# Performance work log

Hardware: AMD Instinct MI355X
Metric: run time of the kernel (lower is better)

The kernel has to match this reference:

```python
import jax, jax.numpy as jnp
import numpy as np

B, C, L, MID, HID, OUT, K = 4096, 6, 1024, 512, 512, 256, 5
EPS = 1e-5


def _bn_eval(x, g, b, m, v):
    # BatchNorm1d eval mode on (B, C, T): normalize per channel with running stats
    inv = g / jnp.sqrt(v + EPS)
    return (x - m[None, :, None]) * inv[None, :, None] + b[None, :, None]


def setup_inputs() -> dict:
    key = jax.random.key(0)
    ks = jax.random.split(key, 12)
    s_in = 1.0 / np.sqrt(L)
    s_hid = 1.0 / np.sqrt(HID)
    inp = {
        "x": jax.random.normal(ks[0], (B, C, L), jnp.float32),
        # k stacked self-attention branches (two Linear(L, MID) each)
        "aW1": jax.random.normal(ks[1], (K, L, MID), jnp.float32) * s_in,
        "ab1": jnp.zeros((K, MID), jnp.float32),
        "aW2": jax.random.normal(ks[2], (K, L, MID), jnp.float32) * s_in,
        "ab2": jnp.zeros((K, MID), jnp.float32),
        # linearExchangeLayer: Linear(K*C, C)
        "linW": jax.random.normal(ks[3], (K * C, C), jnp.float32) / np.sqrt(K * C),
        "linb": jnp.zeros((C,), jnp.float32),
        # GraphConvolution weights
        "gW1": jax.random.normal(ks[4], (L, HID), jnp.float32) * s_in,
        "gb1": jnp.zeros((HID,), jnp.float32),
        "gW2": jax.random.normal(ks[5], (HID, OUT), jnp.float32) * s_hid,
        "gb2": jnp.zeros((OUT,), jnp.float32),
        # PReLU (single shared parameter, torch default 0.25)
        "prelu_a": jnp.array(0.25, jnp.float32),
        # BatchNorm1d params + running stats (eval mode)
        "bn1_g": jnp.ones((C,), jnp.float32),
        "bn1_b": jnp.zeros((C,), jnp.float32),
        "bn1_m": jnp.zeros((C,), jnp.float32),
        "bn1_v": jnp.ones((C,), jnp.float32),
        "bn2_g": jnp.ones((C,), jnp.float32),
        "bn2_b": jnp.zeros((C,), jnp.float32),
        "bn2_m": jnp.zeros((C,), jnp.float32),
        "bn2_v": jnp.ones((C,), jnp.float32),
    }
    return inp


def reference(x, aW1, ab1, aW2, ab2, linW, linb, gW1, gb1, gW2, gb2,
              prelu_a, bn1_g, bn1_b, bn1_m, bn1_v, bn2_g, bn2_b, bn2_m, bn2_v):
    b, c, l = x.shape
    k = aW1.shape[0]
    # --- multi-head attention adjacency: (b, c, c) ---
    q = jnp.einsum('bcl,klm->bkcm', x, aW1) + ab1[None, :, None, :]
    kv = jnp.einsum('bcl,klm->bkcm', x, aW2) + ab2[None, :, None, :]
    scores = jax.nn.softmax(jnp.einsum('bkcm,bkdm->bkcd', q, kv), axis=-1)
    # concat heads along last dim: (b, c, k*c)
    cat = scores.transpose(0, 2, 1, 3).reshape(b, c, k * c)
    A = jax.nn.softmax(cat @ linW + linb, axis=-1)  # (b, c, c)
    # --- GraphConvolution 1 (dropout identity in eval) ---
    h = jnp.einsum('bcd,bdh->bch', A, x @ gW1) + gb1
    # PReLU then BatchNorm1d
    h = jnp.where(h >= 0, h, prelu_a * h)
    h = _bn_eval(h, bn1_g, bn1_b, bn1_m, bn1_v)
    # --- GraphConvolution 2 ---
    out = jnp.einsum('bcd,bdh->bch', A, h @ gW2) + gb2
    out = _bn_eval(out, bn2_g, bn2_b, bn2_m, bn2_v)
    return out
```

## Files before the change

### kernel.cpp

```cpp
#include <hip/hip_runtime.h>
#include <hip/hip_bf16.h>


using bf16 = __hip_bfloat16;
using s16x8 = __attribute__((ext_vector_type(8))) short;
using f32x4 = __attribute__((ext_vector_type(4))) float;

#define AS1(p) ((__attribute__((address_space(1))) void*)((void*)(p)))
#define AS3(p) ((__attribute__((address_space(3))) void*)(p))

#if defined(__has_builtin)
#if __has_builtin(__builtin_amdgcn_global_load_lds)
#define HAVE_GLL 1
#endif
#endif

__device__ __forceinline__ float s2f(short s) {
  union { unsigned int u; float f; } c;
  c.u = ((unsigned int)(unsigned short)s) << 16;
  return c.f;
}
__device__ __forceinline__ short f2s(float x) {
  bf16 b = __float2bfloat16(x);
  short s;
  __builtin_memcpy(&s, &b, 2);
  return s;
}

struct GJob {
  const bf16* Bt;
  const float* bias;
  int boff;
  bf16* out;
};

__global__ void cvt_f32_bf16(const float* __restrict__ in, bf16* __restrict__ out, int n8) {
  int i = blockIdx.x * blockDim.x + threadIdx.x;
  if (i >= n8) return;
  float4 p0 = ((const float4*)in)[i * 2];
  float4 p1 = ((const float4*)in)[i * 2 + 1];
  s16x8 v;
  v[0] = f2s(p0.x); v[1] = f2s(p0.y); v[2] = f2s(p0.z); v[3] = f2s(p0.w);
  v[4] = f2s(p1.x); v[5] = f2s(p1.y); v[6] = f2s(p1.z); v[7] = f2s(p1.w);
  ((s16x8*)out)[i] = v;
}

__global__ void transpose_f2b(const float* __restrict__ in, bf16* __restrict__ out,
                              int R, int C) {
  __shared__ short tile[32][33];
  const float* src = in + (size_t)blockIdx.z * R * C;
  short* dst = (short*)out + (size_t)blockIdx.z * R * C;
  int r0 = blockIdx.x * 32, c0 = blockIdx.y * 32;
  int tx = threadIdx.x, ty = threadIdx.y;
#pragma unroll
  for (int i = 0; i < 4; ++i)
    tile[ty + i * 8][tx] = f2s(src[(size_t)(r0 + ty + i * 8) * C + c0 + tx]);
  __syncthreads();
#pragma unroll
  for (int i = 0; i < 4; ++i)
    dst[(size_t)(c0 + ty + i * 8) * R + r0 + tx] = tile[tx][ty + i * 8];
}

template <int AF32>
__global__ __launch_bounds__(256) void gemm_bt(
    const void* __restrict__ Ag,
    const bf16* __restrict__ Bt0, const bf16* __restrict__ Bt1,
    const float* __restrict__ bias0, const float* __restrict__ bias1, int boff,
    bf16* __restrict__ out0, bf16* __restrict__ out1,
    int M, int N, int K) {
  const bf16* Bt = (blockIdx.z == 0) ? Bt0 : Bt1;
  const float* bias = (blockIdx.z == 0) ? bias0 : bias1;
  bf16* Cg = (blockIdx.z == 0) ? out0 : out1;

  __shared__ short lA[128 * 32];
  __shared__ short lB[128 * 32];

  const int tid = threadIdx.x;
  const int lane = tid & 63, w = tid >> 6;
  const int wr = w >> 1, wc = w & 1;
  const int l16 = lane & 15, quad = lane >> 4;
  const int lrow = lane >> 2;
  const int scol = (((lane & 3) ^ ((lane >> 3) & 3)) * 8);

  const size_t rm0 = (size_t)blockIdx.x * 128;
  const size_t cn0 = (size_t)blockIdx.y * 128;

  f32x4 acc[4][4];
#pragma unroll
  for (int i = 0; i < 4; ++i)
#pragma unroll
    for (int j = 0; j < 4; ++j) acc[i][j] = (f32x4){0.f, 0.f, 0.f, 0.f};

  for (int kb = 0; kb < K; kb += 32) {
#pragma unroll
    for (int t = 0; t < 2; ++t) {
      int chunk = w * 2 + t;
      int row = chunk * 16 + lrow;
      const bf16* gb = Bt + (cn0 + row) * (size_t)K + kb + scol;
#ifdef HAVE_GLL
      __builtin_amdgcn_global_load_lds(AS1(gb), AS3(lB + chunk * 512), 16, 0, 0);
#else
      *(s16x8*)(lB + chunk * 512 + lane * 8) = *(const s16x8*)gb;
#endif
      if (AF32) {
        const float* ga = (const float*)Ag + (rm0 + row) * (size_t)K + kb + scol;
        float4 p0 = *(const float4*)ga;
        float4 p1 = *(const float4*)(ga + 4);
        s16x8 v;
        v[0] = f2s(p0.x); v[1] = f2s(p0.y); v[2] = f2s(p0.z); v[3] = f2s(p0.w);
        v[4] = f2s(p1.x); v[5] = f2s(p1.y); v[6] = f2s(p1.z); v[7] = f2s(p1.w);
        *(s16x8*)(lA + chunk * 512 + lane * 8) = v;
      } else {
        const bf16* ga = (const bf16*)Ag + (rm0 + row) * (size_t)K + kb + scol;
#ifdef HAVE_GLL
        __builtin_amdgcn_global_load_lds(AS1(ga), AS3(lA + chunk * 512), 16, 0, 0);
#else
        *(s16x8*)(lA + chunk * 512 + lane * 8) = *(const s16x8*)ga;
#endif
      }
    }
    __syncthreads();

    const int q2 = (quad ^ ((l16 >> 1) & 3)) * 8;
    s16x8 af[4], bfv[4];
#pragma unroll
    for (int i = 0; i < 4; ++i) {
      af[i] = *(const s16x8*)(lA + (wr * 64 + i * 16 + l16) * 32 + q2);
      bfv[i] = *(const s16x8*)(lB + (wc * 64 + i * 16 + l16) * 32 + q2);
    }
#pragma unroll
    for (int i = 0; i < 4; ++i)
#pragma unroll
      for (int j = 0; j < 4; ++j)
        acc[i][j] = __builtin_amdgcn_mfma_f32_16x16x32_bf16(af[i], bfv[j], acc[i][j], 0, 0, 0);
    __syncthreads();
  }

#pragma unroll
  for (int j = 0; j < 4; ++j) {
    size_t col = cn0 + wc * 64 + j * 16 + l16;
    float bv = bias ? bias[boff + col] : 0.f;
#pragma unroll
    for (int i = 0; i < 4; ++i) {
      size_t rowb = rm0 + wr * 64 + i * 16 + quad * 4;
#pragma unroll
      for (int r = 0; r < 4; ++r) {
        float v = acc[i][j][r] + bv;
        Cg[(rowb + r) * (size_t)N + col] = __float2bfloat16(v);
      }
    }
  }
}

__global__ __launch_bounds__(512, 2) void gemm256_8ph(
    const bf16* __restrict__ A,
    GJob j0, GJob j1, GJob j2, GJob j3,
    int M, int N, int K) {
  const GJob j = (blockIdx.z == 0) ? j0 : (blockIdx.z == 1) ? j1
               : (blockIdx.z == 2) ? j2 : j3;
  const bf16* Bt = j.Bt;
  const float* bias = j.bias;
  const int boff = j.boff;
  bf16* Cg = j.out;

  __shared__ __attribute__((aligned(16))) short ldsS[65536];

  const int tid = threadIdx.x;
  const int w = tid >> 6, l = tid & 63;
  const int l16 = l & 15, quad = l >> 4;
  const int wr = w >> 2, wc = w & 3;

  const size_t rm0 = (size_t)blockIdx.x * 256;
  const size_t cn0 = (size_t)blockIdx.y * 256;

  const int colS = ((l & 7) ^ (l >> 3)) * 8;
  const int rowS = w * 16 + (l >> 3);
  const short* pAs = (const short*)A + (rm0 + rowS) * (size_t)K + colS;
  const short* pBs = (const short*)Bt + (cn0 + rowS) * (size_t)K + colS;

  const int u0 = (quad ^ (l16 & 7)) * 8;
  const int u1 = ((quad + 4) ^ (l16 & 7)) * 8;

  f32x4 acc[8][4];
#pragma unroll
  for (int i = 0; i < 8; ++i)
#pragma unroll
    for (int j2i = 0; j2i < 4; ++j2i) acc[i][j2i] = (f32x4){0.f, 0.f, 0.f, 0.f};

  s16x8 af[4][2], bf0[2][2], bf1[2][2];

  const int T = K >> 6;

#ifdef HAVE_GLL
#define SA(BUF, H, KB) do {                                                          \
    __builtin_amdgcn_global_load_lds(AS1(pAs + (size_t)((H) * 128) * K + (KB)),      \
        AS3(ldsS + (BUF) * 32768 + (H) * 8192 + w * 1024), 16, 0, 0);                \
    __builtin_amdgcn_global_load_lds(AS1(pAs + (size_t)((H) * 128 + 8) * K + (KB)),  \
        AS3(ldsS + (BUF) * 32768 + (H) * 8192 + w * 1024 + 512), 16, 0, 0);          \
  } while (0)
#define SB(BUF, H, KB) do {                                                          \
    __builtin_amdgcn_global_load_lds(AS1(pBs + (size_t)((H) * 128) * K + (KB)),      \
        AS3(ldsS + (BUF) * 32768 + 16384 + (H) * 8192 + w * 1024), 16, 0, 0);        \
    __builtin_amdgcn_global_load_lds(AS1(pBs + (size_t)((H) * 128 + 8) * K + (KB)),  \
        AS3(ldsS + (BUF) * 32768 + 16384 + (H) * 8192 + w * 1024 + 512), 16, 0, 0);  \
  } while (0)
#else
#define SA(BUF, H, KB) do {                                                          \
    *(s16x8*)(ldsS + (BUF) * 32768 + (H) * 8192 + w * 1024 + l * 8) =                \
        *(const s16x8*)(pAs + (size_t)((H) * 128) * K + (KB));                       \
    *(s16x8*)(ldsS + (BUF) * 32768 + (H) * 8192 + w * 1024 + 512 + l * 8) =          \
        *(const s16x8*)(pAs + (size_t)((H) * 128 + 8) * K + (KB));                   \
  } while (0)
#define SB(BUF, H, KB) do {                                                          \
    *(s16x8*)(ldsS + (BUF) * 32768 + 16384 + (H) * 8192 + w * 1024 + l * 8) =        \
        *(const s16x8*)(pBs + (size_t)((H) * 128) * K + (KB));                       \
    *(s16x8*)(ldsS + (BUF) * 32768 + 16384 + (H) * 8192 + w * 1024 + 512 + l * 8) =  \
        *(const s16x8*)(pBs + (size_t)((H) * 128 + 8) * K + (KB));                   \
  } while (0)
#endif

#define LDA(BUF, MH) do {                                                            \
    _Pragma("unroll") for (int i = 0; i < 4; ++i) {                                  \
      const short* bse = ldsS + (BUF) * 32768 + wr * 8192 + (MH) * 4096 +            \
                         i * 1024 + l16 * 64;                                        \
      af[i][0] = *(const s16x8*)(bse + u0);                                          \
      af[i][1] = *(const s16x8*)(bse + u1);                                          \
    }                                                                                \
  } while (0)

#define LDB(BUF, NH, DST) do {                                                       \
    _Pragma("unroll") for (int n = 0; n < 2; ++n) {                                  \
      const short* bse = ldsS + (BUF) * 32768 + 16384 + (wc >> 1) * 8192 +           \
                         (wc & 1) * 4096 + (NH) * 2048 + n * 1024 + l16 * 64;        \
      DST[n][0] = *(const s16x8*)(bse + u0);                                         \
      DST[n][1] = *(const s16x8*)(bse + u1);                                         \
    }                                                                                \
  } while (0)

#define MFMAQ(MH, NH, BSET) do {                                                     \
    _Pragma("unroll") for (int i = 0; i < 4; ++i)                                    \
      _Pragma("unroll") for (int n = 0; n < 2; ++n) {                                \
        acc[(MH) * 4 + i][(NH) * 2 + n] = __builtin_amdgcn_mfma_f32_16x16x32_bf16(   \
            af[i][0], BSET[n][0], acc[(MH) * 4 + i][(NH) * 2 + n], 0, 0, 0);         \
        acc[(MH) * 4 + i][(NH) * 2 + n] = __builtin_amdgcn_mfma_f32_16x16x32_bf16(   \
            af[i][1], BSET[n][1], acc[(MH) * 4 + i][(NH) * 2 + n], 0, 0, 0);         \
      }                                                                              \
  } while (0)

#define BARX() asm volatile("s_barrier" ::: "memory")
#define LGKM0() do { asm volatile("s_waitcnt lgkmcnt(0)" ::: "memory");              \
                     __builtin_amdgcn_sched_barrier(0); } while (0)
#define VM6() do { asm volatile("s_waitcnt vmcnt(6)" ::: "memory");                  \
                   __builtin_amdgcn_sched_barrier(0); } while (0)

#define TILE_STEP(BUF, t) do {                                                       \
    const int kN_ = ((t) + 1 < T ? (t) + 1 : T - 1) << 6;                            \
    const int k2_ = ((t) + 2 < T ? (t) + 2 : T - 1) << 6;                            \
               \
    LDA(BUF, 0); LDB(BUF, 0, bf0); LDB(BUF, 1, bf1);                                 \
    SA((BUF) ^ 1, 1, kN_);                                                           \
    BARX(); LGKM0();                                                                 \
    __builtin_amdgcn_s_setprio(1); MFMAQ(0, 0, bf0); __builtin_amdgcn_s_setprio(0);  \
    BARX();                                                                          \
                        \
    SB(BUF, 0, k2_);                                                                 \
    BARX();                                                                          \
    __builtin_amdgcn_s_setprio(1); MFMAQ(0, 1, bf1); __builtin_amdgcn_s_setprio(0);  \
    BARX();                                                                          \
                                               \
    LDA(BUF, 1);                                                                     \
    SB(BUF, 1, k2_);                                                                 \
    BARX(); LGKM0();                                                                 \
    __builtin_amdgcn_s_setprio(1); MFMAQ(1, 1, bf1); __builtin_amdgcn_s_setprio(0);  \
    BARX();                                                                          \
                         \
    SA(BUF, 0, k2_);                                                                 \
    VM6();                                                                           \
    BARX();                                                                          \
    __builtin_amdgcn_s_setprio(1); MFMAQ(1, 0, bf0); __builtin_amdgcn_s_setprio(0);  \
    BARX();                                                                          \
  } while (0)

  {
    const int k1_ = (T > 1 ? 1 : 0) << 6;
    SB(0, 0, 0); SB(0, 1, 0); SA(0, 0, 0); SA(0, 1, 0);
    SB(1, 0, k1_); SB(1, 1, k1_); SA(1, 0, k1_);
    VM6();
    BARX();
  }

  for (int t = 0; t < T; t += 2) {
    TILE_STEP(0, t);
    TILE_STEP(1, t + 1);
  }

#pragma unroll
  for (int jj = 0; jj < 4; ++jj) {
    size_t col = cn0 + wc * 64 + jj * 16 + l16;
    float bv = bias ? bias[boff + col] : 0.f;
#pragma unroll
    for (int i = 0; i < 8; ++i) {
      size_t rowb = rm0 + wr * 128 + i * 16 + quad * 4;
#pragma unroll
      for (int r = 0; r < 4; ++r) {
        Cg[(rowb + r) * (size_t)N + col] = __float2bfloat16(acc[i][jj][r] + bv);
      }
    }
  }
#undef SA
#undef SB
#undef LDA
#undef LDB
#undef MFMAQ
#undef BARX
#undef LGKM0
#undef VM6
#undef TILE_STEP
}

__global__ __launch_bounds__(256) void scores_mfma2(
    const bf16* __restrict__ Q0, const bf16* __restrict__ KV0,
    const bf16* __restrict__ Q1, const bf16* __restrict__ KV1,
    float* __restrict__ S, int head0) {
  const int h = blockIdx.y;
  const bf16* Q = h ? Q1 : Q0;
  const bf16* KV = h ? KV1 : KV0;
  const int head = head0 + h;

  const int tid = threadIdx.x;
  const int lane = tid & 63, w = tid >> 6;
  const int l16 = lane & 15, quad = lane >> 4;
  const int b0 = (blockIdx.x * 4 + w) * 2;

  int gr = (l16 < 8) ? (b0 * 6 + l16) : ((b0 + 1) * 6 + (l16 - 8));
  if (gr > 24575) gr = 24575;

  const short* qrow = (const short*)Q + (size_t)gr * 512 + quad * 8;
  const short* krow = (const short*)KV + (size_t)gr * 512 + quad * 8;

  f32x4 acc = (f32x4){0.f, 0.f, 0.f, 0.f};
#pragma unroll
  for (int kk = 0; kk < 16; ++kk) {
    s16x8 a = *(const s16x8*)(qrow + kk * 32);
    s16x8 b = *(const s16x8*)(krow + kk * 32);
    acc = __builtin_amdgcn_mfma_f32_16x16x32_bf16(a, b, acc, 0, 0, 0);
  }

  if (l16 < 6) {
#pragma unroll
    for (int r = 0; r < 4; ++r) {
      int m = quad * 4 + r;
      if (m < 6)
        S[((size_t)b0 * 5 + head) * 36 + m * 6 + l16] = acc[r];
    }
  } else if (l16 >= 8 && l16 < 14) {
#pragma unroll
    for (int r = 0; r < 4; ++r) {
      int m = quad * 4 + r;
      if (m >= 8 && m < 14)
        S[((size_t)(b0 + 1) * 5 + head) * 36 + (m - 8) * 6 + (l16 - 8)] = acc[r];
    }
  }
}

__global__ void batch_mid_kernel(const float* __restrict__ S, const bf16* __restrict__ XG,
                                 const float* __restrict__ linW, const float* __restrict__ linb,
                                 const float* __restrict__ gb1, const float* __restrict__ prelu,
                                 const float* __restrict__ g1, const float* __restrict__ b1,
                                 const float* __restrict__ m1, const float* __restrict__ v1,
                                 float* __restrict__ Afull, bf16* __restrict__ H) {
  int b = blockIdx.x, tid = threadIdx.x;
  __shared__ float p[5][6][6];
  __shared__ float Ar[6][6];
  __shared__ float lw[30][6];
  __shared__ float lbv[6];
  __shared__ float sc1[6], sm1[6], sb1[6];

  if (tid < 30) {
    int k = tid / 6, c = tid % 6;
    const float* sp = S + ((size_t)b * 5 + k) * 36 + c * 6;
    float v[6], mx = sp[0];
#pragma unroll
    for (int d = 0; d < 6; ++d) { v[d] = sp[d]; mx = fmaxf(mx, v[d]); }
    float s = 0.f;
#pragma unroll
    for (int d = 0; d < 6; ++d) { v[d] = expf(v[d] - mx); s += v[d]; }
    float inv = 1.f / s;
#pragma unroll
    for (int d = 0; d < 6; ++d) p[k][c][d] = v[d] * inv;
#pragma unroll
    for (int j = 0; j < 6; ++j) lw[tid][j] = linW[tid * 6 + j];
  }
  if (tid < 6) {
    lbv[tid] = linb[tid];
    sc1[tid] = g1[tid] * rsqrtf(v1[tid] + 1e-5f);
    sm1[tid] = m1[tid];
    sb1[tid] = b1[tid];
  }
  __syncthreads();

  if (tid < 6) {
    int c = tid;
    float ap[6];
#pragma unroll
    for (int j = 0; j < 6; ++j) ap[j] = lbv[j];
    for (int k = 0; k < 5; ++k)
#pragma unroll
      for (int d = 0; d < 6; ++d) {
        float pv = p[k][c][d];
#pragma unroll
        for (int j = 0; j < 6; ++j) ap[j] += pv * lw[k * 6 + d][j];
      }
    float mx = ap[0];
#pragma unroll
    for (int j = 1; j < 6; ++j) mx = fmaxf(mx, ap[j]);
    float s = 0.f;
#pragma unroll
    for (int j = 0; j < 6; ++j) { ap[j] = expf(ap[j] - mx); s += ap[j]; }
    float inv = 1.f / s;
#pragma unroll
    for (int j = 0; j < 6; ++j) {
      float a = ap[j] * inv;
      Ar[c][j] = a;
      Afull[(size_t)b * 36 + c * 6 + j] = a;
    }
  }
  __syncthreads();

  float pa = prelu[0];
  for (int col = tid; col < 512; col += 64) {
    float xg[6];
#pragma unroll
    for (int d = 0; d < 6; ++d) xg[d] = s2f(((const short*)XG)[((size_t)b * 6 + d) * 512 + col]);
    float gbv = gb1[col];
#pragma unroll
    for (int c = 0; c < 6; ++c) {
      float h = gbv;
#pragma unroll
      for (int d = 0; d < 6; ++d) h += Ar[c][d] * xg[d];
      h = (h >= 0.f) ? h : pa * h;
      h = (h - sm1[c]) * sc1[c] + sb1[c];
      H[((size_t)b * 6 + c) * 512 + col] = __float2bfloat16(h);
    }
  }
}

__global__ void batch_out_kernel(const float* __restrict__ Afull, const bf16* __restrict__ HW,
                                 const float* __restrict__ gb2,
                                 const float* __restrict__ g2, const float* __restrict__ b2,
                                 const float* __restrict__ m2, const float* __restrict__ v2,
                                 float* __restrict__ out) {
  int b = blockIdx.x, tid = threadIdx.x;
  __shared__ float Ar[36];
  __shared__ float sc[6], sm[6], sb[6];
  if (tid < 36) Ar[tid] = Afull[(size_t)b * 36 + tid];
  if (tid < 6) {
    sc[tid] = g2[tid] * rsqrtf(v2[tid] + 1e-5f);
    sm[tid] = m2[tid];
    sb[tid] = b2[tid];
  }
  __syncthreads();
  for (int col = tid; col < 256; col += 64) {
    float hw[6];
#pragma unroll
    for (int d = 0; d < 6; ++d) hw[d] = s2f(((const short*)HW)[((size_t)b * 6 + d) * 256 + col]);
    float gv = gb2[col];
#pragma unroll
    for (int c = 0; c < 6; ++c) {
      float o = gv;
#pragma unroll
      for (int d = 0; d < 6; ++d) o += Ar[c * 6 + d] * hw[d];
      o = (o - sm[c]) * sc[c] + sb[c];
      out[((size_t)b * 6 + c) * 256 + col] = o;
    }
  }
}

extern "C" void kernel_launch(void* const* d_in, const int* in_sizes, int n_in,
                              void* d_out, int out_size, void* d_ws, size_t ws_size,
                              hipStream_t stream) {
  const float* x    = (const float*)d_in[0];
  const float* aW1  = (const float*)d_in[1];
  const float* ab1  = (const float*)d_in[2];
  const float* aW2  = (const float*)d_in[3];
  const float* ab2  = (const float*)d_in[4];
  const float* linW = (const float*)d_in[5];
  const float* linb = (const float*)d_in[6];
  const float* gW1  = (const float*)d_in[7];
  const float* gb1  = (const float*)d_in[8];
  const float* gW2  = (const float*)d_in[9];
  const float* gb2  = (const float*)d_in[10];
  const float* prelu = (const float*)d_in[11];
  const float* bn1g = (const float*)d_in[12];
  const float* bn1b = (const float*)d_in[13];
  const float* bn1m = (const float*)d_in[14];
  const float* bn1v = (const float*)d_in[15];
  const float* bn2g = (const float*)d_in[16];
  const float* bn2b = (const float*)d_in[17];
  const float* bn2m = (const float*)d_in[18];
  const float* bn2v = (const float*)d_in[19];

  char* ws = (char*)d_ws;
  bf16* W1T  = (bf16*)(ws + 0);
  bf16* W2T  = (bf16*)(ws + 5242880);
  bf16* G1T  = (bf16*)(ws + 10485760);
  bf16* G2T  = (bf16*)(ws + 11534336);
  float* S   = (float*)(ws + 11796480);
  float* Af  = (float*)(ws + 14745600);
  bf16* BufA = (bf16*)(ws + 15335424);
  bf16* BufB = (bf16*)(ws + 40501248);
  bf16* Xb   = (bf16*)(ws + 65667072);
  bf16* BufA2 = (bf16*)(ws + 115998720);
  bf16* BufB2 = (bf16*)(ws + 141164544);
  const bool big  = ws_size >= 115998720ull;
  const bool big2 = ws_size >= 166330368ull;

  dim3 tb(32, 8);
  transpose_f2b<<<dim3(32, 16, 5), tb, 0, stream>>>(aW1, W1T, 1024, 512);
  transpose_f2b<<<dim3(32, 16, 5), tb, 0, stream>>>(aW2, W2T, 1024, 512);
  transpose_f2b<<<dim3(32, 16, 1), tb, 0, stream>>>(gW1, G1T, 1024, 512);
  transpose_f2b<<<dim3(16, 8, 1),  tb, 0, stream>>>(gW2, G2T, 512, 256);
  if (big) cvt_f32_bf16<<<12288, 256, 0, stream>>>(x, Xb, 3145728);

  if (big2) {
    for (int k = 0; k < 4; k += 2) {
      const size_t wo0 = (size_t)k * 524288, wo1 = (size_t)(k + 1) * 524288;
      GJob jq0{W1T + wo0, ab1, k * 512, BufA};
      GJob jk0{W2T + wo0, ab2, k * 512, BufB};
      GJob jq1{W1T + wo1, ab1, (k + 1) * 512, BufA2};
      GJob jk1{W2T + wo1, ab2, (k + 1) * 512, BufB2};
      gemm256_8ph<<<dim3(96, 2, 4), 512, 0, stream>>>(
          Xb, jq0, jk0, jq1, jk1, 24576, 512, 1024);
      scores_mfma2<<<dim3(512, 2), 256, 0, stream>>>(BufA, BufB, BufA2, BufB2, S, k);
    }
    {
      const size_t wo4 = (size_t)4 * 524288;
      GJob jq4{W1T + wo4, ab1, 4 * 512, BufA};
      GJob jk4{W2T + wo4, ab2, 4 * 512, BufB};
      GJob jxg{G1T, nullptr, 0, BufA2};
      gemm256_8ph<<<dim3(96, 2, 3), 512, 0, stream>>>(
          Xb, jq4, jk4, jxg, jxg, 24576, 512, 1024);
      scores_mfma2<<<dim3(512, 1), 256, 0, stream>>>(BufA, BufB, BufA, BufB, S, 4);
    }
    batch_mid_kernel<<<4096, 64, 0, stream>>>(S, BufA2, linW, linb, gb1, prelu,
                                              bn1g, bn1b, bn1m, bn1v, Af, BufB);
  } else {
    for (int k = 0; k < 5; ++k) {
      const bf16* w1 = W1T + (size_t)k * 524288;
      const bf16* w2 = W2T + (size_t)k * 524288;
      if (big) {
        GJob jq{w1, ab1, k * 512, BufA};
        GJob jk{w2, ab2, k * 512, BufB};
        gemm256_8ph<<<dim3(96, 2, 2), 512, 0, stream>>>(
            Xb, jq, jk, jq, jk, 24576, 512, 1024);
      } else {
        gemm_bt<1><<<dim3(192, 4, 2), 256, 0, stream>>>(
            x, w1, w2, ab1, ab2, k * 512, BufA, BufB, 24576, 512, 1024);
      }
      scores_mfma2<<<dim3(512, 1), 256, 0, stream>>>(BufA, BufB, BufA, BufB, S, k);
    }
    if (big) {
      GJob jxg{G1T, nullptr, 0, BufA};
      gemm256_8ph<<<dim3(96, 2, 1), 512, 0, stream>>>(
          Xb, jxg, jxg, jxg, jxg, 24576, 512, 1024);
    } else {
      gemm_bt<1><<<dim3(192, 4, 1), 256, 0, stream>>>(
          x, G1T, G1T, nullptr, nullptr, 0, BufA, BufA, 24576, 512, 1024);
    }
    batch_mid_kernel<<<4096, 64, 0, stream>>>(S, BufA, linW, linb, gb1, prelu,
                                              bn1g, bn1b, bn1m, bn1v, Af, BufB);
  }

  gemm_bt<0><<<dim3(192, 2, 1), 256, 0, stream>>>(
      BufB, G2T, G2T, nullptr, nullptr, 0, BufA, BufA, 24576, 256, 512);

  batch_out_kernel<<<4096, 64, 0, stream>>>(Af, BufA, gb2, bn2g, bn2b, bn2m, bn2v,
                                            (float*)d_out);
}
```

Baseline: 631.5 us.

## Fuse prep kernels and overlap score computation with projection GEMMs

Merges the weight transposes and input conversion into one prep kernel, and adds extra grid z-slices to the big GEMM that compute attention scores for earlier heads while later heads' projections run. With a larger workspace it keeps four Q/KV buffer pairs so that three GEMM launches cover all heads, and it folds the last head's score computation into the batch-mid kernel. The batch kernels now handle four batches per block. The aim is fewer launches and less idle tail time, in exchange for more workspace memory and score work that runs inside the GEMM grid, where it may compete with the GEMM tiles.

```diff
diff --git a/kernel.cpp b/kernel.cpp
--- a/kernel.cpp
+++ b/kernel.cpp
@@ -33,25 +33,52 @@
   int boff;
   bf16* out;
 };
-
-__global__ void cvt_f32_bf16(const float* __restrict__ in, bf16* __restrict__ out, int n8) {
-  int i = blockIdx.x * blockDim.x + threadIdx.x;
-  if (i >= n8) return;
-  float4 p0 = ((const float4*)in)[i * 2];
-  float4 p1 = ((const float4*)in)[i * 2 + 1];
-  s16x8 v;
-  v[0] = f2s(p0.x); v[1] = f2s(p0.y); v[2] = f2s(p0.z); v[3] = f2s(p0.w);
-  v[4] = f2s(p1.x); v[5] = f2s(p1.y); v[6] = f2s(p1.z); v[7] = f2s(p1.w);
-  ((s16x8*)out)[i] = v;
-}
-
-__global__ void transpose_f2b(const float* __restrict__ in, bf16* __restrict__ out,
-                              int R, int C) {
+struct ScJob {
+  const bf16* Q;
+  const bf16* KV;
+  float* S;
+  int head;
+};
+
+__global__ __launch_bounds__(256) void prep_kernel(
+    const float* __restrict__ x, bf16* __restrict__ Xb, int do_cvt,
+    const float* __restrict__ aW1, bf16* __restrict__ W1T,
+    const float* __restrict__ aW2, bf16* __restrict__ W2T,
+    const float* __restrict__ gW1, bf16* __restrict__ G1T,
+    const float* __restrict__ gW2, bf16* __restrict__ G2T) {
+  const int bid = blockIdx.x, tid = threadIdx.x;
+  if (bid < 12288) {
+    if (!do_cvt) return;
+    int i = bid * 256 + tid;
+    float4 p0 = ((const float4*)x)[i * 2];
+    float4 p1 = ((const float4*)x)[i * 2 + 1];
+    s16x8 v;
+    v[0] = f2s(p0.x); v[1] = f2s(p0.y); v[2] = f2s(p0.z); v[3] = f2s(p0.w);
+    v[4] = f2s(p1.x); v[5] = f2s(p1.y); v[6] = f2s(p1.z); v[7] = f2s(p1.w);
+    ((s16x8*)Xb)[i] = v;
+    return;
+  }
+  int r = bid - 12288;
+  const float* src; short* dst; int R, C, bx, by;
+  if (r < 2560) {
+    int z = r >> 9, q = r & 511;
+    src = aW1 + (size_t)z * 524288; dst = (short*)W1T + (size_t)z * 524288;
+    R = 1024; C = 512; bx = q & 31; by = q >> 5;
+  } else if (r < 5120) {
+    r -= 2560;
+    int z = r >> 9, q = r & 511;
+    src = aW2 + (size_t)z * 524288; dst = (short*)W2T + (size_t)z * 524288;
+    R = 1024; C = 512; bx = q & 31; by = q >> 5;
+  } else if (r < 5632) {
+    r -= 5120;
+    src = gW1; dst = (short*)G1T; R = 1024; C = 512; bx = r & 31; by = r >> 5;
+  } else {
+    r -= 5632;
+    src = gW2; dst = (short*)G2T; R = 512; C = 256; bx = r & 15; by = r >> 4;
+  }
   __shared__ short tile[32][33];
-  const float* src = in + (size_t)blockIdx.z * R * C;
-  short* dst = (short*)out + (size_t)blockIdx.z * R * C;
-  int r0 = blockIdx.x * 32, c0 = blockIdx.y * 32;
-  int tx = threadIdx.x, ty = threadIdx.y;
+  const int tx = tid & 31, ty = tid >> 5;
+  const int r0 = bx * 32, c0 = by * 32;
 #pragma unroll
   for (int i = 0; i < 4; ++i)
     tile[ty + i * 8][tx] = f2s(src[(size_t)(r0 + ty + i * 8) * C + c0 + tx]);
@@ -59,6 +86,53 @@
 #pragma unroll
   for (int i = 0; i < 4; ++i)
     dst[(size_t)(c0 + ty + i * 8) * R + r0 + tx] = tile[tx][ty + i * 8];
+}
+
+__device__ __forceinline__ void scores_wave(
+    const bf16* __restrict__ Q, const bf16* __restrict__ KV,
+    float* __restrict__ S, int head, int b0, int lane) {
+  const int l16 = lane & 15, quad = lane >> 4;
+  const int lr0 = (l16 < 8) ? l16 : (l16 - 8);
+  const int lr = (lr0 <= 5) ? lr0 : 5;
+  const int gb = (l16 < 8) ? b0 : (b0 + 1);
+  const int gr = gb * 6 + lr;
+
+  const short* qrow = (const short*)Q + (size_t)gr * 512 + quad * 8;
+  const short* krow = (const short*)KV + (size_t)gr * 512 + quad * 8;
+
+  f32x4 acc = (f32x4){0.f, 0.f, 0.f, 0.f};
+#pragma unroll
+  for (int kk = 0; kk < 16; ++kk) {
+    s16x8 a = *(const s16x8*)(qrow + kk * 32);
+    s16x8 b = *(const s16x8*)(krow + kk * 32);
+    acc = __builtin_amdgcn_mfma_f32_16x16x32_bf16(a, b, acc, 0, 0, 0);
+  }
+
+  if (l16 < 6) {
+#pragma unroll
+    for (int r = 0; r < 4; ++r) {
+      int m = quad * 4 + r;
+      if (m < 6)
+        S[((size_t)b0 * 5 + head) * 36 + m * 6 + l16] = acc[r];
+    }
+  } else if (l16 >= 8 && l16 < 14) {
+#pragma unroll
+    for (int r = 0; r < 4; ++r) {
+      int m = quad * 4 + r;
+      if (m >= 8 && m < 14)
+        S[((size_t)(b0 + 1) * 5 + head) * 36 + (m - 8) * 6 + (l16 - 8)] = acc[r];
+    }
+  }
+}
+
+__global__ __launch_bounds__(256) void scores_mfma2(
+    const bf16* __restrict__ Q0, const bf16* __restrict__ KV0,
+    const bf16* __restrict__ Q1, const bf16* __restrict__ KV1,
+    float* __restrict__ S, int head0) {
+  const int h = blockIdx.y;
+  const int lane = threadIdx.x & 63, w = threadIdx.x >> 6;
+  const int b0 = (blockIdx.x * 4 + w) * 2;
+  scores_wave(h ? Q1 : Q0, h ? KV1 : KV0, S, head0 + h, b0, lane);
 }
 
 template <int AF32>
@@ -155,7 +229,18 @@
 __global__ __launch_bounds__(512, 2) void gemm256_8ph(
     const bf16* __restrict__ A,
     GJob j0, GJob j1, GJob j2, GJob j3,
+    int nzg, ScJob s0, ScJob s1,
     int M, int N, int K) {
+  if ((int)blockIdx.z >= nzg) {
+    ScJob sc = ((int)blockIdx.z == nzg) ? s0 : s1;
+    const int lane = threadIdx.x & 63, w = threadIdx.x >> 6;
+    const int stride = gridDim.x * gridDim.y * 8;
+    const int base = ((int)blockIdx.y * gridDim.x + blockIdx.x) * 8 + w;
+    for (int job = base; job < 2048; job += stride)
+      scores_wave(sc.Q, sc.KV, sc.S, sc.head, job * 2, lane);
+    return;
+  }
+
   const GJob j = (blockIdx.z == 0) ? j0 : (blockIdx.z == 1) ? j1
                : (blockIdx.z == 2) ? j2 : j3;
   const bf16* Bt = j.Bt;
@@ -318,76 +403,22 @@
 #undef TILE_STEP
 }
 
-__global__ __launch_bounds__(256) void scores_mfma2(
-    const bf16* __restrict__ Q0, const bf16* __restrict__ KV0,
-    const bf16* __restrict__ Q1, const bf16* __restrict__ KV1,
-    float* __restrict__ S, int head0) {
-  const int h = blockIdx.y;
-  const bf16* Q = h ? Q1 : Q0;
-  const bf16* KV = h ? KV1 : KV0;
-  const int head = head0 + h;
-
-  const int tid = threadIdx.x;
-  const int lane = tid & 63, w = tid >> 6;
-  const int l16 = lane & 15, quad = lane >> 4;
-  const int b0 = (blockIdx.x * 4 + w) * 2;
-
-  int gr = (l16 < 8) ? (b0 * 6 + l16) : ((b0 + 1) * 6 + (l16 - 8));
-  if (gr > 24575) gr = 24575;
-
-  const short* qrow = (const short*)Q + (size_t)gr * 512 + quad * 8;
-  const short* krow = (const short*)KV + (size_t)gr * 512 + quad * 8;
-
-  f32x4 acc = (f32x4){0.f, 0.f, 0.f, 0.f};
-#pragma unroll
-  for (int kk = 0; kk < 16; ++kk) {
-    s16x8 a = *(const s16x8*)(qrow + kk * 32);
-    s16x8 b = *(const s16x8*)(krow + kk * 32);
-    acc = __builtin_amdgcn_mfma_f32_16x16x32_bf16(a, b, acc, 0, 0, 0);
-  }
-
-  if (l16 < 6) {
-#pragma unroll
-    for (int r = 0; r < 4; ++r) {
-      int m = quad * 4 + r;
-      if (m < 6)
-        S[((size_t)b0 * 5 + head) * 36 + m * 6 + l16] = acc[r];
-    }
-  } else if (l16 >= 8 && l16 < 14) {
-#pragma unroll
-    for (int r = 0; r < 4; ++r) {
-      int m = quad * 4 + r;
-      if (m >= 8 && m < 14)
-        S[((size_t)(b0 + 1) * 5 + head) * 36 + (m - 8) * 6 + (l16 - 8)] = acc[r];
-    }
-  }
-}
-
-__global__ void batch_mid_kernel(const float* __restrict__ S, const bf16* __restrict__ XG,
-                                 const float* __restrict__ linW, const float* __restrict__ linb,
-                                 const float* __restrict__ gb1, const float* __restrict__ prelu,
-                                 const float* __restrict__ g1, const float* __restrict__ b1,
-                                 const float* __restrict__ m1, const float* __restrict__ v1,
-                                 float* __restrict__ Afull, bf16* __restrict__ H) {
-  int b = blockIdx.x, tid = threadIdx.x;
-  __shared__ float p[5][6][6];
-  __shared__ float Ar[6][6];
+__global__ __launch_bounds__(256) void batch_mid4(
+    const float* __restrict__ S, const bf16* __restrict__ XG,
+    const bf16* __restrict__ Q4, const bf16* __restrict__ KV4, int fuse5,
+    const float* __restrict__ linW, const float* __restrict__ linb,
+    const float* __restrict__ gb1, const float* __restrict__ prelu,
+    const float* __restrict__ g1, const float* __restrict__ b1,
+    const float* __restrict__ m1, const float* __restrict__ v1,
+    float* __restrict__ Afull, bf16* __restrict__ H) {
+  const int tid = threadIdx.x, g = tid >> 6, t = tid & 63;
+  const int b = blockIdx.x * 4 + g;
+  __shared__ float p[4][5][6][6];
+  __shared__ float Ar[4][6][6];
   __shared__ float lw[30][6];
-  __shared__ float lbv[6];
-  __shared__ float sc1[6], sm1[6], sb1[6];
+  __shared__ float lbv[6], sc1[6], sm1[6], sb1[6];
 
   if (tid < 30) {
-    int k = tid / 6, c = tid % 6;
-    const float* sp = S + ((size_t)b * 5 + k) * 36 + c * 6;
-    float v[6], mx = sp[0];
-#pragma unroll
-    for (int d = 0; d < 6; ++d) { v[d] = sp[d]; mx = fmaxf(mx, v[d]); }
-    float s = 0.f;
-#pragma unroll
-    for (int d = 0; d < 6; ++d) { v[d] = expf(v[d] - mx); s += v[d]; }
-    float inv = 1.f / s;
-#pragma unroll
-    for (int d = 0; d < 6; ++d) p[k][c][d] = v[d] * inv;
 #pragma unroll
     for (int j = 0; j < 6; ++j) lw[tid][j] = linW[tid * 6 + j];
   }
@@ -397,17 +428,53 @@
     sm1[tid] = m1[tid];
     sb1[tid] = b1[tid];
   }
+  if (fuse5 && t < 36) {
+    int c = t / 6, d = t % 6;
+    const s16x8* qr = (const s16x8*)((const short*)Q4 + ((size_t)b * 6 + c) * 512);
+    const s16x8* kr = (const s16x8*)((const short*)KV4 + ((size_t)b * 6 + d) * 512);
+    float acc = 0.f;
+#pragma unroll 4
+    for (int i = 0; i < 64; ++i) {
+      s16x8 qa = qr[i], kb = kr[i];
+#pragma unroll
+      for (int j = 0; j < 8; ++j) acc += s2f(qa[j]) * s2f(kb[j]);
+    }
+    p[g][4][c][d] = acc;
+  }
   __syncthreads();
 
-  if (tid < 6) {
-    int c = tid;
+  if (t < 30) {
+    int k = t / 6, c = t % 6;
+    float v[6];
+    if (k == 4 && fuse5) {
+#pragma unroll
+      for (int d = 0; d < 6; ++d) v[d] = p[g][4][c][d];
+    } else {
+      const float* sp = S + ((size_t)b * 5 + k) * 36 + c * 6;
+#pragma unroll
+      for (int d = 0; d < 6; ++d) v[d] = sp[d];
+    }
+    float mx = v[0];
+#pragma unroll
+    for (int d = 1; d < 6; ++d) mx = fmaxf(mx, v[d]);
+    float s = 0.f;
+#pragma unroll
+    for (int d = 0; d < 6; ++d) { v[d] = expf(v[d] - mx); s += v[d]; }
+    float inv = 1.f / s;
+#pragma unroll
+    for (int d = 0; d < 6; ++d) p[g][k][c][d] = v[d] * inv;
+  }
+  __syncthreads();
+
+  if (t < 6) {
+    int c = t;
     float ap[6];
 #pragma unroll
     for (int j = 0; j < 6; ++j) ap[j] = lbv[j];
     for (int k = 0; k < 5; ++k)
 #pragma unroll
       for (int d = 0; d < 6; ++d) {
-        float pv = p[k][c][d];
+        float pv = p[g][k][c][d];
 #pragma unroll
         for (int j = 0; j < 6; ++j) ap[j] += pv * lw[k * 6 + d][j];
       }
@@ -421,14 +488,14 @@
 #pragma unroll
     for (int j = 0; j < 6; ++j) {
       float a = ap[j] * inv;
-      Ar[c][j] = a;
+      Ar[g][c][j] = a;
       Afull[(size_t)b * 36 + c * 6 + j] = a;
     }
   }
   __syncthreads();
 
   float pa = prelu[0];
-  for (int col = tid; col < 512; col += 64) {
+  for (int col = t; col < 512; col += 64) {
     float xg[6];
 #pragma unroll
     for (int d = 0; d < 6; ++d) xg[d] = s2f(((const short*)XG)[((size_t)b * 6 + d) * 512 + col]);
@@ -437,7 +504,7 @@
     for (int c = 0; c < 6; ++c) {
       float h = gbv;
 #pragma unroll
-      for (int d = 0; d < 6; ++d) h += Ar[c][d] * xg[d];
+      for (int d = 0; d < 6; ++d) h += Ar[g][c][d] * xg[d];
       h = (h >= 0.f) ? h : pa * h;
       h = (h - sm1[c]) * sc1[c] + sb1[c];
       H[((size_t)b * 6 + c) * 512 + col] = __float2bfloat16(h);
@@ -445,22 +512,24 @@
   }
 }
 
-__global__ void batch_out_kernel(const float* __restrict__ Afull, const bf16* __restrict__ HW,
-                                 const float* __restrict__ gb2,
-                                 const float* __restrict__ g2, const float* __restrict__ b2,
-                                 const float* __restrict__ m2, const float* __restrict__ v2,
-                                 float* __restrict__ out) {
-  int b = blockIdx.x, tid = threadIdx.x;
-  __shared__ float Ar[36];
+__global__ __launch_bounds__(256) void batch_out4(
+    const float* __restrict__ Afull, const bf16* __restrict__ HW,
+    const float* __restrict__ gb2,
+    const float* __restrict__ g2, const float* __restrict__ b2,
+    const float* __restrict__ m2, const float* __restrict__ v2,
+    float* __restrict__ out) {
+  const int tid = threadIdx.x, g = tid >> 6, t = tid & 63;
+  const int b = blockIdx.x * 4 + g;
+  __shared__ float Ar[4][36];
   __shared__ float sc[6], sm[6], sb[6];
-  if (tid < 36) Ar[tid] = Afull[(size_t)b * 36 + tid];
+  if (t < 36) Ar[g][t] = Afull[(size_t)b * 36 + t];
   if (tid < 6) {
     sc[tid] = g2[tid] * rsqrtf(v2[tid] + 1e-5f);
     sm[tid] = m2[tid];
     sb[tid] = b2[tid];
   }
   __syncthreads();
-  for (int col = tid; col < 256; col += 64) {
+  for (int col = t; col < 256; col += 64) {
     float hw[6];
 #pragma unroll
     for (int d = 0; d < 6; ++d) hw[d] = s2f(((const short*)HW)[((size_t)b * 6 + d) * 256 + col]);
@@ -469,7 +538,7 @@
     for (int c = 0; c < 6; ++c) {
       float o = gv;
 #pragma unroll
-      for (int d = 0; d < 6; ++d) o += Ar[c * 6 + d] * hw[d];
+      for (int d = 0; d < 6; ++d) o += Ar[g][c * 6 + d] * hw[d];
       o = (o - sm[c]) * sc[c] + sb[c];
       out[((size_t)b * 6 + c) * 256 + col] = o;
     }
@@ -501,79 +570,98 @@
   const float* bn2v = (const float*)d_in[19];
 
   char* ws = (char*)d_ws;
-  bf16* W1T  = (bf16*)(ws + 0);
-  bf16* W2T  = (bf16*)(ws + 5242880);
-  bf16* G1T  = (bf16*)(ws + 10485760);
-  bf16* G2T  = (bf16*)(ws + 11534336);
-  float* S   = (float*)(ws + 11796480);
-  float* Af  = (float*)(ws + 14745600);
-  bf16* BufA = (bf16*)(ws + 15335424);
-  bf16* BufB = (bf16*)(ws + 40501248);
-  bf16* Xb   = (bf16*)(ws + 65667072);
+  bf16* W1T   = (bf16*)(ws + 0);
+  bf16* W2T   = (bf16*)(ws + 5242880);
+  bf16* G1T   = (bf16*)(ws + 10485760);
+  bf16* G2T   = (bf16*)(ws + 11534336);
+  float* S    = (float*)(ws + 11796480);
+  float* Af   = (float*)(ws + 14745600);
+  bf16* BufA  = (bf16*)(ws + 15335424);
+  bf16* BufB  = (bf16*)(ws + 40501248);
+  bf16* Xb    = (bf16*)(ws + 65667072);
   bf16* BufA2 = (bf16*)(ws + 115998720);
   bf16* BufB2 = (bf16*)(ws + 141164544);
+  bf16* BufA3 = (bf16*)(ws + 166330368);
+  bf16* BufB3 = (bf16*)(ws + 191496192);
+  bf16* BufA4 = (bf16*)(ws + 216662016);
+  bf16* BufB4 = (bf16*)(ws + 241827840);
   const bool big  = ws_size >= 115998720ull;
   const bool big2 = ws_size >= 166330368ull;
-
-  dim3 tb(32, 8);
-  transpose_f2b<<<dim3(32, 16, 5), tb, 0, stream>>>(aW1, W1T, 1024, 512);
-  transpose_f2b<<<dim3(32, 16, 5), tb, 0, stream>>>(aW2, W2T, 1024, 512);
-  transpose_f2b<<<dim3(32, 16, 1), tb, 0, stream>>>(gW1, G1T, 1024, 512);
-  transpose_f2b<<<dim3(16, 8, 1),  tb, 0, stream>>>(gW2, G2T, 512, 256);
-  if (big) cvt_f32_bf16<<<12288, 256, 0, stream>>>(x, Xb, 3145728);
-
-  if (big2) {
+  const bool big3 = ws_size >= 266993664ull;
+
+  prep_kernel<<<18048, 256, 0, stream>>>(x, Xb, big ? 1 : 0,
+                                         aW1, W1T, aW2, W2T, gW1, G1T, gW2, G2T);
+
+  ScJob scz{nullptr, nullptr, nullptr, 0};
+
+  if (big3) {
+    GJob q0{W1T, ab1, 0, BufA},                 k0{W2T, ab2, 0, BufB};
+    GJob q1{W1T + 524288, ab1, 512, BufA2},     k1{W2T + 524288, ab2, 512, BufB2};
+    gemm256_8ph<<<dim3(96, 2, 4), 512, 0, stream>>>(
+        Xb, q0, k0, q1, k1, 4, scz, scz, 24576, 512, 1024);
+    GJob q2{W1T + 2 * 524288, ab1, 1024, BufA3}, k2{W2T + 2 * 524288, ab2, 1024, BufB3};
+    GJob q3{W1T + 3 * 524288, ab1, 1536, BufA4}, k3{W2T + 3 * 524288, ab2, 1536, BufB4};
+    ScJob sA{BufA, BufB, S, 0}, sB{BufA2, BufB2, S, 1};
+    gemm256_8ph<<<dim3(96, 2, 6), 512, 0, stream>>>(
+        Xb, q2, k2, q3, k3, 4, sA, sB, 24576, 512, 1024);
+    GJob q4{W1T + 4 * 524288, ab1, 2048, BufA}, k4{W2T + 4 * 524288, ab2, 2048, BufB};
+    GJob jxg{G1T, nullptr, 0, BufA2};
+    ScJob sC{BufA3, BufB3, S, 2}, sD{BufA4, BufB4, S, 3};
+    gemm256_8ph<<<dim3(96, 2, 5), 512, 0, stream>>>(
+        Xb, q4, k4, jxg, jxg, 3, sC, sD, 24576, 512, 1024);
+    batch_mid4<<<1024, 256, 0, stream>>>(S, BufA2, BufA, BufB, 1, linW, linb,
+                                         gb1, prelu, bn1g, bn1b, bn1m, bn1v,
+                                         Af, BufB2);
+  } else if (big2) {
     for (int k = 0; k < 4; k += 2) {
-      const size_t wo0 = (size_t)k * 524288, wo1 = (size_t)(k + 1) * 524288;
-      GJob jq0{W1T + wo0, ab1, k * 512, BufA};
-      GJob jk0{W2T + wo0, ab2, k * 512, BufB};
-      GJob jq1{W1T + wo1, ab1, (k + 1) * 512, BufA2};
-      GJob jk1{W2T + wo1, ab2, (k + 1) * 512, BufB2};
+      GJob qa{W1T + (size_t)k * 524288, ab1, k * 512, BufA};
+      GJob ka{W2T + (size_t)k * 524288, ab2, k * 512, BufB};
+      GJob qb{W1T + (size_t)(k + 1) * 524288, ab1, (k + 1) * 512, BufA2};
+      GJob kb{W2T + (size_t)(k + 1) * 524288, ab2, (k + 1) * 512, BufB2};
       gemm256_8ph<<<dim3(96, 2, 4), 512, 0, stream>>>(
-          Xb, jq0, jk0, jq1, jk1, 24576, 512, 1024);
+          Xb, qa, ka, qb, kb, 4, scz, scz, 24576, 512, 1024);
       scores_mfma2<<<dim3(512, 2), 256, 0, stream>>>(BufA, BufB, BufA2, BufB2, S, k);
     }
-    {
-      const size_t wo4 = (size_t)4 * 524288;
-      GJob jq4{W1T + wo4, ab1, 4 * 512, BufA};
-      GJob jk4{W2T + wo4, ab2, 4 * 512, BufB};
-      GJob jxg{G1T, nullptr, 0, BufA2};
-      gemm256_8ph<<<dim3(96, 2, 3), 512, 0, stream>>>(
-          Xb, jq4, jk4, jxg, jxg, 24576, 512, 1024);
-      scores_mfma2<<<dim3(512, 1), 256, 0, stream>>>(BufA, BufB, BufA, BufB, S, 4);
-    }
-    batch_mid_kernel<<<4096, 64, 0, stream>>>(S, BufA2, linW, linb, gb1, prelu,
-                                              bn1g, bn1b, bn1m, bn1v, Af, BufB);
+    GJob q4{W1T + 4 * 524288, ab1, 2048, BufA}, k4{W2T + 4 * 524288, ab2, 2048, BufB};
+    GJob jxg{G1T, nullptr, 0, BufA2};
+    gemm256_8ph<<<dim3(96, 2, 3), 512, 0, stream>>>(
+        Xb, q4, k4, jxg, jxg, 4, scz, scz, 24576, 512, 1024);
+    batch_mid4<<<1024, 256, 0, stream>>>(S, BufA2, BufA, BufB, 1, linW, linb,
+                                         gb1, prelu, bn1g, bn1b, bn1m, bn1v,
+                                         Af, BufB2);
+  } else if (big) {
+    for (int k = 0; k < 5; ++k) {
+      GJob q{W1T + (size_t)k * 524288, ab1, k * 512, BufA};
+      GJob kk{W2T + (size_t)k * 524288, ab2, k * 512, BufB};
+      gemm256_8ph<<<dim3(96, 2, 2), 512, 0, stream>>>(
+          Xb, q, kk, q, kk, 4, scz, scz, 24576, 512, 1024);
+      scores_mfma2<<<dim3(512, 1), 256, 0, stream>>>(BufA, BufB, BufA, BufB, S, k);
+    }
+    GJob jxg{G1T, nullptr, 0, BufA};
+    gemm256_8ph<<<dim3(96, 2, 1), 512, 0, stream>>>(
+        Xb, jxg, jxg, jxg, jxg, 4, scz, scz, 24576, 512, 1024);
+    batch_mid4<<<1024, 256, 0, stream>>>(S, BufA, BufA, BufA, 0, linW, linb,
+                                         gb1, prelu, bn1g, bn1b, bn1m, bn1v,
+                                         Af, BufB);
   } else {
     for (int k = 0; k < 5; ++k) {
       const bf16* w1 = W1T + (size_t)k * 524288;
       const bf16* w2 = W2T + (size_t)k * 524288;
-      if (big) {
-        GJob jq{w1, ab1, k * 512, BufA};
-        GJob jk{w2, ab2, k * 512, BufB};
-        gemm256_8ph<<<dim3(96, 2, 2), 512, 0, stream>>>(
-            Xb, jq, jk, jq, jk, 24576, 512, 1024);
-      } else {
-        gemm_bt<1><<<dim3(192, 4, 2), 256, 0, stream>>>(
-            x, w1, w2, ab1, ab2, k * 512, BufA, BufB, 24576, 512, 1024);
-      }
+      gemm_bt<1><<<dim3(192, 4, 2), 256, 0, stream>>>(
+          x, w1, w2, ab1, ab2, k * 512, BufA, BufB, 24576, 512, 1024);
       scores_mfma2<<<dim3(512, 1), 256, 0, stream>>>(BufA, BufB, BufA, BufB, S, k);
     }
-    if (big) {
-      GJob jxg{G1T, nullptr, 0, BufA};
-      gemm256_8ph<<<dim3(96, 2, 1), 512, 0, stream>>>(
-          Xb, jxg, jxg, jxg, jxg, 24576, 512, 1024);
-    } else {
-      gemm_bt<1><<<dim3(192, 4, 1), 256, 0, stream>>>(
-          x, G1T, G1T, nullptr, nullptr, 0, BufA, BufA, 24576, 512, 1024);
-    }
-    batch_mid_kernel<<<4096, 64, 0, stream>>>(S, BufA, linW, linb, gb1, prelu,
-                                              bn1g, bn1b, bn1m, bn1v, Af, BufB);
-  }
-
+    gemm_bt<1><<<dim3(192, 4, 1), 256, 0, stream>>>(
+        x, G1T, G1T, nullptr, nullptr, 0, BufA, BufA, 24576, 512, 1024);
+    batch_mid4<<<1024, 256, 0, stream>>>(S, BufA, BufA, BufA, 0, linW, linb,
+                                         gb1, prelu, bn1g, bn1b, bn1m, bn1v,
+                                         Af, BufB);
+  }
+
+  bf16* Hbuf = big2 ? BufB2 : BufB;
   gemm_bt<0><<<dim3(192, 2, 1), 256, 0, stream>>>(
-      BufB, G2T, G2T, nullptr, nullptr, 0, BufA, BufA, 24576, 256, 512);
-
-  batch_out_kernel<<<4096, 64, 0, stream>>>(Af, BufA, gb2, bn2g, bn2b, bn2m, bn2v,
-                                            (float*)d_out);
-}
+      Hbuf, G2T, G2T, nullptr, nullptr, 0, BufA, BufA, 24576, 256, 512);
+
+  batch_out4<<<1024, 256, 0, stream>>>(Af, BufA, gb2, bn2g, bn2b, bn2m, bn2v,
+                                       (float*)d_out);
+}
```

Result: no change. 636.6 us (+0.8%).
